# Kernel optimization log

Hardware: AMD Instinct MI355X
Metric: run time of the kernel (lower is better)

## Reference

```python
import jax, jax.numpy as jnp
import numpy as np

B, S, H = 2, 2048, 2048
NH, NKV, HD = 16, 8, 128        # head_dim = H // NH
WINDOW = 1024                    # sliding window size
THETA = 100000.0                 # rope_theta (RotaryEmbedding base)


def setup_inputs() -> dict:
    key = jax.random.key(0)
    ks = jax.random.split(key, 5)
    hidden = jax.random.normal(ks[0], (B, S, H), jnp.float32)
    # fused QKV projection: [H, NH*HD + 2*NKV*HD]
    W_pack = jax.random.normal(ks[1], (H, NH * HD + 2 * NKV * HD), jnp.float32) * (H ** -0.5)
    W_o = jax.random.normal(ks[2], (NH * HD, H), jnp.float32) * ((NH * HD) ** -0.5)
    # per-KV-head 2-tap causal conv weights, softmax-normalized (as in nn.Parameter init)
    conv_k = jax.nn.softmax(jax.random.normal(ks[3], (NKV, 2), jnp.float32), axis=-1)
    conv_v = jax.nn.softmax(jax.random.normal(ks[4], (NKV, 2), jnp.float32), axis=-1)
    return {"hidden": hidden, "W_pack": W_pack, "W_o": W_o, "conv_k": conv_k, "conv_v": conv_v}


def _rope(x, cos, sin):
    # x: (b, s, h, d); cos/sin: (s, d//2); non-interleaved (rotate-half) form
    d2 = x.shape[-1] // 2
    x1, x2 = x[..., :d2], x[..., d2:]
    c = cos[None, :, None, :]
    s = sin[None, :, None, :]
    return jnp.concatenate([x1 * c - x2 * s, x2 * c + x1 * s], axis=-1)


def _causal_conv2(x, w):
    # x: (b, s, kv, d); w: (kv, 2). out[t] = w0*x[t-1] + w1*x[t], zero-padded at t=0
    x_prev = jnp.pad(x, ((0, 0), (1, 0), (0, 0), (0, 0)))[:, :-1]
    return w[None, None, :, 0:1] * x_prev + w[None, None, :, 1:2] * x


def reference(hidden, W_pack, W_o, conv_k, conv_v):
    b, s, _ = hidden.shape
    qkv = hidden @ W_pack                                  # (b, s, NH*HD + 2*NKV*HD)
    q = qkv[..., : NH * HD].reshape(b, s, NH, HD)
    k = qkv[..., NH * HD : NH * HD + NKV * HD].reshape(b, s, NKV, HD)
    v = qkv[..., NH * HD + NKV * HD :].reshape(b, s, NKV, HD)

    inv_freq = 1.0 / (THETA ** (jnp.arange(0, HD, 2, dtype=jnp.float32) / HD))
    freqs = jnp.outer(jnp.arange(s, dtype=jnp.float32), inv_freq)  # (s, HD/2)
    cos, sin = jnp.cos(freqs), jnp.sin(freqs)
    q = _rope(q, cos, sin)
    k = _rope(k, cos, sin)

    # learned 2-tap causal conv mixing adjacent K/V states, per KV head
    k = _causal_conv2(k, conv_k)
    v = _causal_conv2(v, conv_v)

    # GQA: repeat kv heads to match query heads
    group = NH // NKV
    k = jnp.repeat(k, group, axis=2)  # (b, s, NH, HD)
    v = jnp.repeat(v, group, axis=2)

    scores = jnp.einsum('bqhd,bkhd->bhqk', q, k) / jnp.sqrt(jnp.float32(HD))
    i = jnp.arange(s)[:, None]
    j = jnp.arange(s)[None, :]
    mask = (j <= i) & (i - j < WINDOW)  # causal sliding-window mask
    scores = jnp.where(mask[None, None], scores, jnp.finfo(scores.dtype).min)
    probs = jax.nn.softmax(scores, axis=-1)
    out = jnp.einsum('bhqk,bkhd->bqhd', probs, v).reshape(b, s, NH * HD)
    return out @ W_o
```

## Files before the change

### kernel.cpp

```cpp
#include <hip/hip_runtime.h>

#define DI __device__ __forceinline__

typedef unsigned short u16;
typedef __attribute__((ext_vector_type(8))) short s16x8;
typedef __attribute__((ext_vector_type(8))) unsigned short u16x8;
typedef __attribute__((ext_vector_type(4))) float f32x4;
typedef __attribute__((ext_vector_type(16))) float f32x16;

DI u16 f2bf(float x) {
  union { float f; unsigned u; } a; a.f = x;
  unsigned r = a.u + 0x7FFFu + ((a.u >> 16) & 1u);
  return (u16)(r >> 16);
}
DI float bf2f(u16 u) {
  union { unsigned u; float f; } a; a.u = ((unsigned)u) << 16;
  return a.f;
}
DI void gload16(const void* g, void* l) {
  __builtin_amdgcn_global_load_lds(
      (const __attribute__((address_space(1))) unsigned int*)g,
      (__attribute__((address_space(3))) unsigned int*)l, 16, 0, 0);
}
DI f32x4 mfma16(s16x8 a, s16x8 b, f32x4 c) {
  return __builtin_amdgcn_mfma_f32_16x16x32_bf16(a, b, c, 0, 0, 0);
}
DI f32x16 mfma32(s16x8 a, s16x8 b, f32x16 c) {
  return __builtin_amdgcn_mfma_f32_32x32x16_bf16(a, b, c, 0, 0, 0);
}

DI void store4(u16* p, f32x4 v) {
  union { u16 u[4]; unsigned long long ll; } o;
  o.u[0] = f2bf(v[0]); o.u[1] = f2bf(v[1]); o.u[2] = f2bf(v[2]); o.u[3] = f2bf(v[3]);
  *(unsigned long long*)p = o.ll;
}
DI void store4(float* p, f32x4 v) { *(f32x4*)p = v; }

#define SBAR() asm volatile("s_barrier" ::: "memory")

__global__ __launch_bounds__(256) void prep_kernel(
    const float* __restrict__ hidden, const float* __restrict__ W_pack,
    const float* __restrict__ W_o, u16* __restrict__ hA, u16* __restrict__ wpT,
    u16* __restrict__ woT, float* __restrict__ cosT, float* __restrict__ sinT) {
  int bi = blockIdx.x;
  int t = threadIdx.x;
  if (bi < 4096) {
    int i = bi * 256 + t;
    const float4* p = (const float4*)hidden + (size_t)i * 2;
    float4 a = p[0], b = p[1];
    u16x8 o;
    o[0] = f2bf(a.x); o[1] = f2bf(a.y); o[2] = f2bf(a.z); o[3] = f2bf(a.w);
    o[4] = f2bf(b.x); o[5] = f2bf(b.y); o[6] = f2bf(b.z); o[7] = f2bf(b.w);
    *((u16x8*)hA + i) = o;
  } else if (bi < 7168) {
    const float* W; u16* Wt; int R, C, c0, r0;
    if (bi < 6144) {
      int idx = bi - 4096;
      W = W_pack; Wt = wpT; R = 2048; C = 4096;
      c0 = (idx & 63) * 64; r0 = (idx >> 6) * 64;
    } else {
      int idx = bi - 6144;
      W = W_o; Wt = woT; R = 2048; C = 2048;
      c0 = (idx & 31) * 64; r0 = (idx >> 5) * 64;
    }
    __shared__ u16 tile[64][65];
#pragma unroll
    for (int i = 0; i < 16; ++i) {
      int flat = i * 256 + t;
      int r = flat >> 6, c = flat & 63;
      tile[r][c] = f2bf(W[(size_t)(r0 + r) * C + (c0 + c)]);
    }
    __syncthreads();
#pragma unroll
    for (int i = 0; i < 16; ++i) {
      int flat = i * 256 + t;
      int c = flat >> 6, r = flat & 63;
      Wt[(size_t)(c0 + c) * R + (r0 + r)] = tile[r][c];
    }
  } else {
    int i = (bi - 7168) * 256 + t;
    int s = i >> 6, d = i & 63;
    float inv = expf(-(float)d * (11.5129254649702295f / 64.f));
    float f = (float)s * inv;
    cosT[i] = cosf(f);
    sinT[i] = sinf(f);
  }
}

__global__ __launch_bounds__(512, 2) void gemm_ring_kernel(
    const u16* __restrict__ A, const u16* __restrict__ Bt, u16* __restrict__ C,
    int M, int N, int K) {
  constexpr int BSZ = 32768;
  __shared__ __align__(16) char lds[4 * BSZ];
  int nwg = gridDim.x, bid = blockIdx.x;
  int cpx = nwg >> 3;
  int swz = (bid & 7) * cpx + (bid >> 3);
  int ntn = N >> 8;
  int bm = swz / ntn, bn = swz - bm * ntn;
  int m0 = bm << 8, n0 = bn << 8;
  int t = threadIdx.x, w = t >> 6, l = t & 63;
  int wm = w >> 2, wn = w & 3;
  int NT = K >> 5;

  unsigned srcA[2], srcB[2];
  unsigned scol = (unsigned)(((t & 3) ^ ((t >> 3) & 3)) << 4);
#pragma unroll
  for (int u = 0; u < 2; ++u) {
    srcA[u] = (unsigned)(m0 + u * 128 + (t >> 2)) * (unsigned)(K * 2) + scol;
    srcB[u] = (unsigned)(n0 + u * 128 + (t >> 2)) * (unsigned)(K * 2) + scol;
  }
  unsigned dstT = (unsigned)(t * 16);
  const char* Ab = (const char*)A;
  const char* Bb = (const char*)Bt;

#define STAGE(tile) do { int _t = (tile); if (_t < NT) {                        \
    char* _bb = lds + (size_t)(_t & 3) * BSZ;                                    \
    unsigned _k = (unsigned)_t * 64u;                                            \
    gload16(Ab + (size_t)(srcA[0] + _k), _bb + dstT);                            \
    gload16(Ab + (size_t)(srcA[1] + _k), _bb + 8192 + dstT);                     \
    gload16(Bb + (size_t)(srcB[0] + _k), _bb + 16384 + dstT);                    \
    gload16(Bb + (size_t)(srcB[1] + _k), _bb + 24576 + dstT);                    \
  } } while (0)

  int lanemix = ((l & 15) << 6) + ((((l >> 4) ^ ((l >> 1) & 3))) << 4);

  f32x4 acc[8][4] = {};
  s16x8 af[8], bfr[4];

  STAGE(0); STAGE(1); STAGE(2);
  asm volatile("s_waitcnt vmcnt(8)" ::: "memory");
  SBAR();

  for (int tt = 0; tt < NT; ++tt) {
    char* buf = lds + (size_t)(tt & 3) * BSZ;
    const char* Ard = buf + wm * 8192 + lanemix;
    const char* Brd = buf + 16384 + wn * 4096 + lanemix;
    STAGE(tt + 3);
#pragma unroll
    for (int mf = 0; mf < 8; ++mf) af[mf] = *(const s16x8*)(Ard + mf * 1024);
#pragma unroll
    for (int nf = 0; nf < 4; ++nf) bfr[nf] = *(const s16x8*)(Brd + nf * 1024);
    __builtin_amdgcn_s_setprio(1);
#pragma unroll
    for (int mf = 0; mf < 8; ++mf)
#pragma unroll
      for (int nf = 0; nf < 4; ++nf)
        acc[mf][nf] = mfma16(bfr[nf], af[mf], acc[mf][nf]);
    __builtin_amdgcn_s_setprio(0);
    if (tt + 1 < NT) {
      if (tt + 3 < NT)      asm volatile("s_waitcnt vmcnt(8)" ::: "memory");
      else if (tt + 2 < NT) asm volatile("s_waitcnt vmcnt(4)" ::: "memory");
      else                  asm volatile("s_waitcnt vmcnt(0)" ::: "memory");
      SBAR();
    }
  }
#undef STAGE

#pragma unroll
  for (int mf = 0; mf < 8; ++mf) {
    int row = m0 + wm * 128 + mf * 16 + (l & 15);
    u16* crow = C + (size_t)row * N + n0 + wn * 64 + (l >> 4) * 4;
#pragma unroll
    for (int nf = 0; nf < 4; ++nf) store4(crow + nf * 16, acc[mf][nf]);
  }
}

__global__ __launch_bounds__(512, 2) void gemm8pn_kernel(
    const u16* __restrict__ A, const u16* __restrict__ Bt, float* __restrict__ C,
    int M, int N, int K) {
  __shared__ __align__(16) char lds[98304];
  int nwg = gridDim.x;
  int bid = blockIdx.x;
  int cpx = nwg >> 3;
  int swz = (bid & 7) * cpx + (bid >> 3);
  int ntn = N >> 7;
  int bm = swz / ntn, bn = swz - bm * ntn;
  int m0 = bm << 8, n0 = bn << 7;
  int t = threadIdx.x, w = t >> 6, l = t & 63;
  int wm = w >> 2, wn = w & 3;
  int NT = K >> 6;

  unsigned offA[4], offB[2];
  int cA[4], cB[2];
#pragma unroll
  for (int u = 0; u < 4; ++u) {
    int c = u * 8 + w;
    cA[u] = c;
    int d = c * 1024 + l * 16;
    int s = d ^ ((((d >> 7) & 7)) << 4);
    offA[u] = (unsigned)(m0 + (s >> 7)) * (unsigned)(K * 2) + (unsigned)(s & 127);
  }
#pragma unroll
  for (int u = 0; u < 2; ++u) {
    int c = u * 8 + w;
    cB[u] = c;
    int d = c * 1024 + l * 16;
    int s = d ^ ((((d >> 7) & 7)) << 4);
    offB[u] = (unsigned)(n0 + (s >> 7)) * (unsigned)(K * 2) + (unsigned)(s & 127);
  }
  const char* Ab = (const char*)A;
  const char* Bb = (const char*)Bt;

#define STG_A(tile, u) do { int _t = (tile); if (_t < NT) {                    \
    gload16(Ab + (size_t)(offA[u] + (unsigned)_t * 128u),                       \
            lds + (_t & 1) * 49152 + cA[u] * 1024); } } while (0)
#define STG_B(tile, u) do { int _t = (tile); if (_t < NT) {                    \
    gload16(Bb + (size_t)(offB[u] + (unsigned)_t * 128u),                       \
            lds + (_t & 1) * 49152 + 32768 + cB[u] * 1024); } } while (0)

  int lanemix = ((l & 15) << 7) + ((((l >> 4) << 4) ^ ((l & 7) << 4)));
  int lanemix1 = lanemix ^ 64;

  f32x4 acc[8][2] = {};
  s16x8 af[4][2], bf0[2], bf1[2];

  STG_A(0, 0); STG_A(0, 1); STG_A(0, 2); STG_A(0, 3); STG_B(0, 0); STG_B(0, 1);
  STG_A(1, 0); STG_A(1, 1); STG_A(1, 2); STG_A(1, 3); STG_B(1, 0); STG_B(1, 1);
  asm volatile("s_waitcnt vmcnt(6)" ::: "memory");
  SBAR();

  for (int tt = 0; tt < NT; ++tt) {
    const char* ldsA = lds + (tt & 1) * 49152;
    const char* ldsB = ldsA + 32768;
    const char* Ard0 = ldsA + (wm << 14) + lanemix;
    const char* Ard1 = ldsA + (wm << 14) + lanemix1;
    const char* Brd0 = ldsB + (wn << 12) + lanemix;
    const char* Brd1 = ldsB + (wn << 12) + lanemix1;

#pragma unroll
    for (int mf = 0; mf < 4; ++mf) {
      af[mf][0] = *(const s16x8*)(Ard0 + mf * 2048);
      af[mf][1] = *(const s16x8*)(Ard1 + mf * 2048);
    }
    bf0[0] = *(const s16x8*)(Brd0);
    bf0[1] = *(const s16x8*)(Brd1);
    SBAR();
    __builtin_amdgcn_s_setprio(1);
#pragma unroll
    for (int mf = 0; mf < 4; ++mf) {
      acc[mf][0] = mfma16(bf0[0], af[mf][0], acc[mf][0]);
      acc[mf][0] = mfma16(bf0[1], af[mf][1], acc[mf][0]);
    }
    __builtin_amdgcn_s_setprio(0);
    SBAR();

    bf1[0] = *(const s16x8*)(Brd0 + 2048);
    bf1[1] = *(const s16x8*)(Brd1 + 2048);
    STG_A(tt + 2, 0); STG_A(tt + 2, 2);
    SBAR();
    __builtin_amdgcn_s_setprio(1);
#pragma unroll
    for (int mf = 0; mf < 4; ++mf) {
      acc[mf][1] = mfma16(bf1[0], af[mf][0], acc[mf][1]);
      acc[mf][1] = mfma16(bf1[1], af[mf][1], acc[mf][1]);
    }
    __builtin_amdgcn_s_setprio(0);
    SBAR();

#pragma unroll
    for (int mf = 0; mf < 4; ++mf) {
      af[mf][0] = *(const s16x8*)(Ard0 + (mf + 4) * 2048);
      af[mf][1] = *(const s16x8*)(Ard1 + (mf + 4) * 2048);
    }
    STG_B(tt + 2, 0); STG_B(tt + 2, 1);
    SBAR();
    __builtin_amdgcn_s_setprio(1);
#pragma unroll
    for (int mf = 0; mf < 4; ++mf) {
      acc[mf + 4][0] = mfma16(bf0[0], af[mf][0], acc[mf + 4][0]);
      acc[mf + 4][0] = mfma16(bf0[1], af[mf][1], acc[mf + 4][0]);
    }
    __builtin_amdgcn_s_setprio(0);
    SBAR();

    STG_A(tt + 2, 1); STG_A(tt + 2, 3);
    SBAR();
    __builtin_amdgcn_s_setprio(1);
#pragma unroll
    for (int mf = 0; mf < 4; ++mf) {
      acc[mf + 4][1] = mfma16(bf1[0], af[mf][0], acc[mf + 4][1]);
      acc[mf + 4][1] = mfma16(bf1[1], af[mf][1], acc[mf + 4][1]);
    }
    __builtin_amdgcn_s_setprio(0);
    if (tt < NT - 2) asm volatile("s_waitcnt vmcnt(6)" ::: "memory");
    else             asm volatile("s_waitcnt vmcnt(0)" ::: "memory");
    SBAR();
  }
#undef STG_A
#undef STG_B

#pragma unroll
  for (int mf = 0; mf < 8; ++mf) {
    int row = m0 + wm * 128 + mf * 16 + (l & 15);
    float* crow = C + (size_t)row * N + n0 + wn * 32 + (l >> 4) * 4;
#pragma unroll
    for (int nf = 0; nf < 2; ++nf) store4(crow + nf * 16, acc[mf][nf]);
  }
}

__global__ void rcvt_kernel(const u16* __restrict__ qkv, const float* __restrict__ cosT,
                            const float* __restrict__ sinT, const float* __restrict__ convk,
                            const float* __restrict__ convv,
                            u16* __restrict__ qb, u16* __restrict__ kb,
                            u16* __restrict__ vt) {
  int t = threadIdx.x;
  if (blockIdx.x < 4096) {
    const float qs = 0.08838834764831845f;
    int row = blockIdx.x;
    int b = row >> 11, s = row & 2047;
    const u16* qr = qkv + (size_t)row * 4096;
    u16* qo = qb + (size_t)row * 2048;
#pragma unroll
    for (int i = 0; i < 4; ++i) {
      int p = i * 256 + t;
      int h = p >> 6, d = p & 63;
      float x1 = bf2f(qr[h * 128 + d]), x2 = bf2f(qr[h * 128 + 64 + d]);
      float c = cosT[s * 64 + d], sn = sinT[s * 64 + d];
      qo[h * 128 + d] = f2bf((x1 * c - x2 * sn) * qs);
      qo[h * 128 + 64 + d] = f2bf((x2 * c + x1 * sn) * qs);
    }
    const u16* kr = qr + 2048;
#pragma unroll
    for (int i = 0; i < 2; ++i) {
      int p = i * 256 + t;
      int h = p >> 6, d = p & 63;
      float c = cosT[s * 64 + d], sn = sinT[s * 64 + d];
      float x1 = bf2f(kr[h * 128 + d]), x2 = bf2f(kr[h * 128 + 64 + d]);
      float r1 = x1 * c - x2 * sn, r2 = x2 * c + x1 * sn;
      float p1 = 0.f, p2 = 0.f;
      if (s > 0) {
        const u16* kp = kr - 4096;
        float cp = cosT[(s - 1) * 64 + d], sp = sinT[(s - 1) * 64 + d];
        float y1 = bf2f(kp[h * 128 + d]), y2 = bf2f(kp[h * 128 + 64 + d]);
        p1 = y1 * cp - y2 * sp;
        p2 = y2 * cp + y1 * sp;
      }
      float w0 = convk[h * 2], w1 = convk[h * 2 + 1];
      size_t o = (((size_t)b * 8 + h) * 2048 + s) * 128;
      kb[o + d] = f2bf(w0 * p1 + w1 * r1);
      kb[o + 64 + d] = f2bf(w0 * p2 + w1 * r2);
    }
  } else {
    __shared__ u16 lt[128][72];
    int idx = blockIdx.x - 4096;
    int st = idx & 31, bh = idx >> 5;
    int b = bh >> 3, h = bh & 7;
    int s0 = st * 64;
    float w0 = convv[h * 2], w1 = convv[h * 2 + 1];
#pragma unroll
    for (int i = 0; i < 32; ++i) {
      int flat = i * 256 + t;
      int sl = flat >> 7, d = flat & 127;
      int s = s0 + sl;
      int row = b * 2048 + s;
      float x = bf2f(qkv[(size_t)row * 4096 + 3072 + h * 128 + d]);
      float xp = (s > 0) ? bf2f(qkv[(size_t)(row - 1) * 4096 + 3072 + h * 128 + d]) : 0.f;
      lt[d][sl] = f2bf(w0 * xp + w1 * x);
    }
    __syncthreads();
#pragma unroll
    for (int i = 0; i < 32; ++i) {
      int flat = i * 256 + t;
      int d = flat >> 6, sl = flat & 63;
      vt[((size_t)(b * 8 + h) * 128 + d) * 2048 + s0 + sl] = lt[d][sl];
    }
  }
}

__global__ __launch_bounds__(256, 2) void attn2_kernel(
    const u16* __restrict__ qb, const u16* __restrict__ kbuf, const u16* __restrict__ vt,
    u16* __restrict__ ao) {
  __shared__ __align__(16) char lds[65536];
  int qt = blockIdx.x, bh = blockIdx.y;
  int b = bh >> 4, h = bh & 15, kh = h >> 1;
  int t = threadIdx.x, w = t >> 6, l = t & 63;
  int i0 = qt * 128;
  int qbase = i0 + w * 32;
  int lq = l & 31, hi = l >> 5;
  int xorc = (l & 7) << 4;
  const char* Kg = (const char*)(kbuf + (size_t)(b * 8 + kh) * 2048 * 128);
  const char* Vg = (const char*)(vt + (size_t)(b * 8 + kh) * 128 * 2048);

  s16x8 qf[8];
  {
    const u16* qp = qb + ((size_t)(b * 2048 + qbase + lq)) * 2048 + h * 128 + 8 * hi;
#pragma unroll
    for (int kc = 0; kc < 8; ++kc) qf[kc] = *(const s16x8*)(qp + kc * 16);
  }

  unsigned ksrc[4], vsrc[4], kdst[4], vdst[4];
#pragma unroll
  for (int i = 0; i < 4; ++i) {
    int c = w * 4 + i;
    int row = c * 4 + (l >> 4);
    int colb = (l & 15) * 16;
    ksrc[i] = (unsigned)(row * 256 + (colb ^ ((row & 7) << 4)));
    kdst[i] = (unsigned)(c * 1024);
    int d = c * 8 + (l >> 3);
    int cb2 = (l & 7) * 16;
    vsrc[i] = (unsigned)(d * 4096 + (cb2 ^ ((d & 7) << 4)));
    vdst[i] = (unsigned)(16384 + c * 1024);
  }

#define STAGEKV(tile, buf) do { int _j2 = (tile) << 6;                          \
    char* _lb = lds + ((buf) << 15);                                             \
    const char* _ks = Kg + (size_t)_j2 * 256;                                    \
    const char* _vs = Vg + (size_t)_j2 * 2;                                      \
    gload16(_ks + ksrc[0], _lb + kdst[0]); gload16(_vs + vsrc[0], _lb + vdst[0]);\
    gload16(_ks + ksrc[1], _lb + kdst[1]); gload16(_vs + vsrc[1], _lb + vdst[1]);\
    gload16(_ks + ksrc[2], _lb + kdst[2]); gload16(_vs + vsrc[2], _lb + vdst[2]);\
    gload16(_ks + ksrc[3], _lb + kdst[3]); gload16(_vs + vsrc[3], _lb + vdst[3]);\
  } while (0)

  int lo = i0 - 1023; if (lo < 0) lo = 0;
  int tk0 = lo >> 6, tk1 = (i0 + 127) >> 6;

  f32x16 acco[4] = {};
  float ls0 = 0.f, ls1 = 0.f, ls2 = 0.f, ls3 = 0.f;

  int cur = 0;
  STAGEKV(tk0, 0);
  asm volatile("s_waitcnt vmcnt(0)" ::: "memory");
  SBAR();

  for (int tk = tk0; tk <= tk1; ++tk) {
    int j0 = tk << 6;
    if (tk < tk1) STAGEKV(tk + 1, cur ^ 1);
    bool relevant = (j0 <= qbase + 31) && (j0 + 63 >= qbase - 1023);
    if (relevant) {
      const char* Kl = lds + (cur << 15);
      const char* Vl = Kl + 16384;
      const char* Krow = Kl + lq * 256;
      f32x16 ps0 = {}, ps1 = {};
      __builtin_amdgcn_s_setprio(1);
#pragma unroll
      for (int kc = 0; kc < 8; ++kc) {
        s16x8 kf = *(const s16x8*)(Krow + ((kc * 32 + hi * 16) ^ xorc));
        ps0 = mfma32(kf, qf[kc], ps0);
      }
#pragma unroll
      for (int kc = 0; kc < 8; ++kc) {
        s16x8 kf = *(const s16x8*)(Krow + 8192 + ((kc * 32 + hi * 16) ^ xorc));
        ps1 = mfma32(kf, qf[kc], ps1);
      }
      __builtin_amdgcn_s_setprio(0);
      bool domask = (j0 + 63 > qbase) || (qbase + 31 - j0 >= 1024);
      int di0 = qbase + lq - j0;
      float pe[32];
#pragma unroll
      for (int r = 0; r < 16; ++r) {
        float s0 = ps0[r], s1 = ps1[r];
        if (domask) {
          int crow = (r & 3) + 8 * (r >> 2) + 4 * hi;
          if ((unsigned)(di0 - crow) >= 1024u) s0 = -1e30f;
          if ((unsigned)(di0 - 32 - crow) >= 1024u) s1 = -1e30f;
        }
        float e0 = __expf(s0), e1 = __expf(s1);
        pe[r] = e0; pe[16 + r] = e1;
        if ((r & 3) == 0) { ls0 += e0 + e1; }
        else if ((r & 3) == 1) { ls1 += e0 + e1; }
        else if ((r & 3) == 2) { ls2 += e0 + e1; }
        else { ls3 += e0 + e1; }
      }
      unsigned pk[16];
#pragma unroll
      for (int p = 0; p < 16; ++p) {
        asm("v_cvt_pk_bf16_f32 %0, %1, %2" : "=v"(pk[p]) : "v"(pe[2 * p]), "v"(pe[2 * p + 1]));
      }
      s16x8 pa[4];
#pragma unroll
      for (int ks = 0; ks < 4; ++ks) {
        int base = (ks >> 1) * 8 + (ks & 1) * 4;
        unsigned keep0 = hi ? pk[base + 2] : pk[base + 0];
        unsigned keep1 = hi ? pk[base + 3] : pk[base + 1];
        unsigned send0 = hi ? pk[base + 0] : pk[base + 2];
        unsigned send1 = hi ? pk[base + 1] : pk[base + 3];
        unsigned recv0 = (unsigned)__shfl_xor((int)send0, 32);
        unsigned recv1 = (unsigned)__shfl_xor((int)send1, 32);
        union { unsigned u[4]; s16x8 v; } pu;
        pu.u[0] = hi ? recv0 : keep0;
        pu.u[1] = hi ? recv1 : keep1;
        pu.u[2] = hi ? keep0 : recv0;
        pu.u[3] = hi ? keep1 : recv1;
        pa[ks] = pu.v;
      }
      __builtin_amdgcn_s_setprio(1);
#pragma unroll
      for (int db = 0; db < 4; ++db) {
        const char* Vrow = Vl + db * 4096 + lq * 128;
#pragma unroll
        for (int ks = 0; ks < 4; ++ks) {
          s16x8 vf = *(const s16x8*)(Vrow + ((ks * 32 + hi * 16) ^ xorc));
          acco[db] = mfma32(pa[ks], vf, acco[db]);
        }
      }
      __builtin_amdgcn_s_setprio(0);
    }
    asm volatile("s_waitcnt vmcnt(0)" ::: "memory");
    SBAR();
    cur ^= 1;
  }
#undef STAGEKV

  float lrow = (ls0 + ls1) + (ls2 + ls3);
  float lt2 = lrow + __shfl_xor(lrow, 32);
  float rinv = 1.f / lt2;
#pragma unroll
  for (int r = 0; r < 16; ++r) {
    int qidx = (r & 3) + 8 * (r >> 2) + 4 * hi;
    float rv = __shfl(rinv, qidx);
    int i = qbase + qidx;
    u16* orow = ao + ((size_t)(b * 2048 + i)) * 2048 + h * 128 + lq;
#pragma unroll
    for (int db = 0; db < 4; ++db)
      orow[db * 32] = f2bf(acco[db][r] * rv);
  }
}

extern "C" void kernel_launch(void* const* d_in, const int* in_sizes, int n_in,
                              void* d_out, int out_size, void* d_ws, size_t ws_size,
                              hipStream_t stream) {
  (void)in_sizes; (void)n_in; (void)out_size; (void)ws_size;
  const float* hidden = (const float*)d_in[0];
  const float* W_pack = (const float*)d_in[1];
  const float* W_o    = (const float*)d_in[2];
  const float* conv_k = (const float*)d_in[3];
  const float* conv_v = (const float*)d_in[4];

  char* ws = (char*)d_ws;
  const size_t MB = 1u << 20;
  u16* hA    = (u16*)(ws + 0);
  u16* wpT   = (u16*)(ws + 16 * MB);
  u16* woT   = (u16*)(ws + 32 * MB);
  u16* qkv   = (u16*)(ws + 40 * MB);
  u16* qb    = (u16*)(ws + 72 * MB);
  u16* kbuf  = (u16*)(ws + 88 * MB);
  u16* vtb   = (u16*)(ws + 96 * MB);
  float* cosT = (float*)(ws + 104 * MB);
  float* sinT = (float*)(ws + 104 * MB + 524288);
  u16* attnb = qkv;

  prep_kernel<<<7680, 256, 0, stream>>>(hidden, W_pack, W_o, hA, wpT, woT, cosT, sinT);
  gemm_ring_kernel<<<256, 512, 0, stream>>>(hA, wpT, qkv, 4096, 4096, 2048);
  rcvt_kernel<<<4608, 256, 0, stream>>>(qkv, cosT, sinT, conv_k, conv_v, qb, kbuf, vtb);
  attn2_kernel<<<dim3(16, 32), 256, 0, stream>>>(qb, kbuf, vtb, attnb);
  gemm8pn_kernel<<<256, 512, 0, stream>>>(attnb, woT, (float*)d_out,
                                          4096, 2048, 2048);
}
```

Baseline: 191.0 us.

## Fuse Q RoPE into attention load and use triple-buffered output GEMM

Result: no change. 192.3 us (+0.7%).

```diff
diff --git a/kernel.cpp b/kernel.cpp
--- a/kernel.cpp
+++ b/kernel.cpp
@@ -165,12 +165,11 @@
   }
 }
 
-__global__ __launch_bounds__(512, 2) void gemm8pn_kernel(
+__global__ __launch_bounds__(512, 2) void gemm2r_kernel(
     const u16* __restrict__ A, const u16* __restrict__ Bt, float* __restrict__ C,
     int M, int N, int K) {
-  __shared__ __align__(16) char lds[98304];
-  int nwg = gridDim.x;
-  int bid = blockIdx.x;
+  __shared__ __align__(16) char lds[3 * 49152];
+  int nwg = gridDim.x, bid = blockIdx.x;
   int cpx = nwg >> 3;
   int swz = (bid & 7) * cpx + (bid >> 3);
   int ntn = N >> 7;
@@ -201,93 +200,59 @@
   const char* Ab = (const char*)A;
   const char* Bb = (const char*)Bt;
 
-#define STG_A(tile, u) do { int _t = (tile); if (_t < NT) {                    \
-    gload16(Ab + (size_t)(offA[u] + (unsigned)_t * 128u),                       \
-            lds + (_t & 1) * 49152 + cA[u] * 1024); } } while (0)
-#define STG_B(tile, u) do { int _t = (tile); if (_t < NT) {                    \
-    gload16(Bb + (size_t)(offB[u] + (unsigned)_t * 128u),                       \
-            lds + (_t & 1) * 49152 + 32768 + cB[u] * 1024); } } while (0)
+#define STG(tile) do { int _t = (tile); if (_t < NT) {                          \
+    char* _bb = lds + (size_t)(_t % 3) * 49152;                                  \
+    unsigned _k = (unsigned)_t * 128u;                                           \
+    gload16(Ab + (size_t)(offA[0] + _k), _bb + cA[0] * 1024);                    \
+    gload16(Ab + (size_t)(offA[1] + _k), _bb + cA[1] * 1024);                    \
+    gload16(Ab + (size_t)(offA[2] + _k), _bb + cA[2] * 1024);                    \
+    gload16(Ab + (size_t)(offA[3] + _k), _bb + cA[3] * 1024);                    \
+    gload16(Bb + (size_t)(offB[0] + _k), _bb + 32768 + cB[0] * 1024);            \
+    gload16(Bb + (size_t)(offB[1] + _k), _bb + 32768 + cB[1] * 1024);            \
+  } } while (0)
 
   int lanemix = ((l & 15) << 7) + ((((l >> 4) << 4) ^ ((l & 7) << 4)));
   int lanemix1 = lanemix ^ 64;
 
   f32x4 acc[8][2] = {};
-  s16x8 af[4][2], bf0[2], bf1[2];
-
-  STG_A(0, 0); STG_A(0, 1); STG_A(0, 2); STG_A(0, 3); STG_B(0, 0); STG_B(0, 1);
-  STG_A(1, 0); STG_A(1, 1); STG_A(1, 2); STG_A(1, 3); STG_B(1, 0); STG_B(1, 1);
+  s16x8 af[8][2], bf0[2], bf1[2];
+
+  STG(0); STG(1);
   asm volatile("s_waitcnt vmcnt(6)" ::: "memory");
   SBAR();
 
   for (int tt = 0; tt < NT; ++tt) {
-    const char* ldsA = lds + (tt & 1) * 49152;
-    const char* ldsB = ldsA + 32768;
-    const char* Ard0 = ldsA + (wm << 14) + lanemix;
-    const char* Ard1 = ldsA + (wm << 14) + lanemix1;
-    const char* Brd0 = ldsB + (wn << 12) + lanemix;
-    const char* Brd1 = ldsB + (wn << 12) + lanemix1;
-
-#pragma unroll
-    for (int mf = 0; mf < 4; ++mf) {
+    char* buf = lds + (size_t)(tt % 3) * 49152;
+    const char* Ard0 = buf + (wm << 14) + lanemix;
+    const char* Ard1 = buf + (wm << 14) + lanemix1;
+    const char* Brd0 = buf + 32768 + (wn << 12) + lanemix;
+    const char* Brd1 = buf + 32768 + (wn << 12) + lanemix1;
+    STG(tt + 2);
+#pragma unroll
+    for (int mf = 0; mf < 8; ++mf) {
       af[mf][0] = *(const s16x8*)(Ard0 + mf * 2048);
       af[mf][1] = *(const s16x8*)(Ard1 + mf * 2048);
     }
     bf0[0] = *(const s16x8*)(Brd0);
     bf0[1] = *(const s16x8*)(Brd1);
-    SBAR();
+    bf1[0] = *(const s16x8*)(Brd0 + 2048);
+    bf1[1] = *(const s16x8*)(Brd1 + 2048);
     __builtin_amdgcn_s_setprio(1);
 #pragma unroll
-    for (int mf = 0; mf < 4; ++mf) {
+    for (int mf = 0; mf < 8; ++mf) {
       acc[mf][0] = mfma16(bf0[0], af[mf][0], acc[mf][0]);
       acc[mf][0] = mfma16(bf0[1], af[mf][1], acc[mf][0]);
-    }
-    __builtin_amdgcn_s_setprio(0);
-    SBAR();
-
-    bf1[0] = *(const s16x8*)(Brd0 + 2048);
-    bf1[1] = *(const s16x8*)(Brd1 + 2048);
-    STG_A(tt + 2, 0); STG_A(tt + 2, 2);
-    SBAR();
-    __builtin_amdgcn_s_setprio(1);
-#pragma unroll
-    for (int mf = 0; mf < 4; ++mf) {
       acc[mf][1] = mfma16(bf1[0], af[mf][0], acc[mf][1]);
       acc[mf][1] = mfma16(bf1[1], af[mf][1], acc[mf][1]);
     }
     __builtin_amdgcn_s_setprio(0);
-    SBAR();
-
-#pragma unroll
-    for (int mf = 0; mf < 4; ++mf) {
-      af[mf][0] = *(const s16x8*)(Ard0 + (mf + 4) * 2048);
-      af[mf][1] = *(const s16x8*)(Ard1 + (mf + 4) * 2048);
-    }
-    STG_B(tt + 2, 0); STG_B(tt + 2, 1);
-    SBAR();
-    __builtin_amdgcn_s_setprio(1);
-#pragma unroll
-    for (int mf = 0; mf < 4; ++mf) {
-      acc[mf + 4][0] = mfma16(bf0[0], af[mf][0], acc[mf + 4][0]);
-      acc[mf + 4][0] = mfma16(bf0[1], af[mf][1], acc[mf + 4][0]);
-    }
-    __builtin_amdgcn_s_setprio(0);
-    SBAR();
-
-    STG_A(tt + 2, 1); STG_A(tt + 2, 3);
-    SBAR();
-    __builtin_amdgcn_s_setprio(1);
-#pragma unroll
-    for (int mf = 0; mf < 4; ++mf) {
-      acc[mf + 4][1] = mfma16(bf1[0], af[mf][0], acc[mf + 4][1]);
-      acc[mf + 4][1] = mfma16(bf1[1], af[mf][1], acc[mf + 4][1]);
-    }
-    __builtin_amdgcn_s_setprio(0);
-    if (tt < NT - 2) asm volatile("s_waitcnt vmcnt(6)" ::: "memory");
-    else             asm volatile("s_waitcnt vmcnt(0)" ::: "memory");
-    SBAR();
-  }
-#undef STG_A
-#undef STG_B
+    if (tt + 1 < NT) {
+      if (tt + 2 < NT) asm volatile("s_waitcnt vmcnt(6)" ::: "memory");
+      else             asm volatile("s_waitcnt vmcnt(0)" ::: "memory");
+      SBAR();
+    }
+  }
+#undef STG
 
 #pragma unroll
   for (int mf = 0; mf < 8; ++mf) {
@@ -301,25 +266,12 @@
 __global__ void rcvt_kernel(const u16* __restrict__ qkv, const float* __restrict__ cosT,
                             const float* __restrict__ sinT, const float* __restrict__ convk,
                             const float* __restrict__ convv,
-                            u16* __restrict__ qb, u16* __restrict__ kb,
-                            u16* __restrict__ vt) {
+                            u16* __restrict__ kb, u16* __restrict__ vt) {
   int t = threadIdx.x;
   if (blockIdx.x < 4096) {
-    const float qs = 0.08838834764831845f;
     int row = blockIdx.x;
     int b = row >> 11, s = row & 2047;
-    const u16* qr = qkv + (size_t)row * 4096;
-    u16* qo = qb + (size_t)row * 2048;
-#pragma unroll
-    for (int i = 0; i < 4; ++i) {
-      int p = i * 256 + t;
-      int h = p >> 6, d = p & 63;
-      float x1 = bf2f(qr[h * 128 + d]), x2 = bf2f(qr[h * 128 + 64 + d]);
-      float c = cosT[s * 64 + d], sn = sinT[s * 64 + d];
-      qo[h * 128 + d] = f2bf((x1 * c - x2 * sn) * qs);
-      qo[h * 128 + 64 + d] = f2bf((x2 * c + x1 * sn) * qs);
-    }
-    const u16* kr = qr + 2048;
+    const u16* kr = qkv + (size_t)row * 4096 + 2048;
 #pragma unroll
     for (int i = 0; i < 2; ++i) {
       int p = i * 256 + t;
@@ -368,8 +320,9 @@
 }
 
 __global__ __launch_bounds__(256, 2) void attn2_kernel(
-    const u16* __restrict__ qb, const u16* __restrict__ kbuf, const u16* __restrict__ vt,
-    u16* __restrict__ ao) {
+    const u16* __restrict__ qkv, const float* __restrict__ cosT,
+    const float* __restrict__ sinT, const u16* __restrict__ kbuf,
+    const u16* __restrict__ vt, u16* __restrict__ ao) {
   __shared__ __align__(16) char lds[65536];
   int qt = blockIdx.x, bh = blockIdx.y;
   int b = bh >> 4, h = bh & 15, kh = h >> 1;
@@ -383,9 +336,32 @@
 
   s16x8 qf[8];
   {
-    const u16* qp = qb + ((size_t)(b * 2048 + qbase + lq)) * 2048 + h * 128 + 8 * hi;
-#pragma unroll
-    for (int kc = 0; kc < 8; ++kc) qf[kc] = *(const s16x8*)(qp + kc * 16);
+    const float qs = 0.08838834764831845f;
+    int srow = qbase + lq;
+    const u16* qp = qkv + ((size_t)(b * 2048 + srow)) * 4096 + h * 128 + 8 * hi;
+    const float* cb = cosT + srow * 64 + 8 * hi;
+    const float* sb = sinT + srow * 64 + 8 * hi;
+#pragma unroll
+    for (int kc = 0; kc < 4; ++kc) {
+      s16x8 vlo = *(const s16x8*)(qp + kc * 16);
+      s16x8 vhi = *(const s16x8*)(qp + 64 + kc * 16);
+      float4 c0 = *(const float4*)(cb + kc * 16);
+      float4 c1 = *(const float4*)(cb + kc * 16 + 4);
+      float4 s0 = *(const float4*)(sb + kc * 16);
+      float4 s1 = *(const float4*)(sb + kc * 16 + 4);
+      float cc[8] = {c0.x, c0.y, c0.z, c0.w, c1.x, c1.y, c1.z, c1.w};
+      float ss[8] = {s0.x, s0.y, s0.z, s0.w, s1.x, s1.y, s1.z, s1.w};
+      u16 ol[8], oh[8];
+#pragma unroll
+      for (int j = 0; j < 8; ++j) {
+        float xl = bf2f(((const u16*)&vlo)[j]);
+        float xh = bf2f(((const u16*)&vhi)[j]);
+        ol[j] = f2bf((xl * cc[j] - xh * ss[j]) * qs);
+        oh[j] = f2bf((xh * cc[j] + xl * ss[j]) * qs);
+      }
+      qf[kc] = *(s16x8*)ol;
+      qf[kc + 4] = *(s16x8*)oh;
+    }
   }
 
   unsigned ksrc[4], vsrc[4], kdst[4], vdst[4];
@@ -533,17 +509,15 @@
   u16* wpT   = (u16*)(ws + 16 * MB);
   u16* woT   = (u16*)(ws + 32 * MB);
   u16* qkv   = (u16*)(ws + 40 * MB);
-  u16* qb    = (u16*)(ws + 72 * MB);
+  u16* attnb = (u16*)(ws + 72 * MB);
   u16* kbuf  = (u16*)(ws + 88 * MB);
   u16* vtb   = (u16*)(ws + 96 * MB);
   float* cosT = (float*)(ws + 104 * MB);
   float* sinT = (float*)(ws + 104 * MB + 524288);
-  u16* attnb = qkv;
 
   prep_kernel<<<7680, 256, 0, stream>>>(hidden, W_pack, W_o, hA, wpT, woT, cosT, sinT);
   gemm_ring_kernel<<<256, 512, 0, stream>>>(hA, wpT, qkv, 4096, 4096, 2048);
-  rcvt_kernel<<<4608, 256, 0, stream>>>(qkv, cosT, sinT, conv_k, conv_v, qb, kbuf, vtb);
-  attn2_kernel<<<dim3(16, 32), 256, 0, stream>>>(qb, kbuf, vtb, attnb);
-  gemm8pn_kernel<<<256, 512, 0, stream>>>(attnb, woT, (float*)d_out,
-                                          4096, 2048, 2048);
-}
+  rcvt_kernel<<<4608, 256, 0, stream>>>(qkv, cosT, sinT, conv_k, conv_v, kbuf, vtb);
+  attn2_kernel<<<dim3(16, 32), 256, 0, stream>>>(qkv, cosT, sinT, kbuf, vtb, attnb);
+  gemm2r_kernel<<<256, 512, 0, stream>>>(attnb, woT, (float*)d_out, 4096, 2048, 2048);
+}
```

## Fuse Q rotary embedding into attention load and use native exp2

Applied to the files above, without the earlier changes.

Measured after the change: 195.9 us. 1.03x slower.

```diff
diff --git a/kernel.cpp b/kernel.cpp
--- a/kernel.cpp
+++ b/kernel.cpp
@@ -27,6 +27,11 @@
 }
 DI f32x16 mfma32(s16x8 a, s16x8 b, f32x16 c) {
   return __builtin_amdgcn_mfma_f32_32x32x16_bf16(a, b, c, 0, 0, 0);
+}
+DI float exp2fast(float x) {
+  float r;
+  asm("v_exp_f32 %0, %1" : "=v"(r) : "v"(x));
+  return r;
 }
 
 DI void store4(u16* p, f32x4 v) {
@@ -301,25 +306,12 @@
 __global__ void rcvt_kernel(const u16* __restrict__ qkv, const float* __restrict__ cosT,
                             const float* __restrict__ sinT, const float* __restrict__ convk,
                             const float* __restrict__ convv,
-                            u16* __restrict__ qb, u16* __restrict__ kb,
-                            u16* __restrict__ vt) {
+                            u16* __restrict__ kb, u16* __restrict__ vt) {
   int t = threadIdx.x;
   if (blockIdx.x < 4096) {
-    const float qs = 0.08838834764831845f;
     int row = blockIdx.x;
     int b = row >> 11, s = row & 2047;
-    const u16* qr = qkv + (size_t)row * 4096;
-    u16* qo = qb + (size_t)row * 2048;
-#pragma unroll
-    for (int i = 0; i < 4; ++i) {
-      int p = i * 256 + t;
-      int h = p >> 6, d = p & 63;
-      float x1 = bf2f(qr[h * 128 + d]), x2 = bf2f(qr[h * 128 + 64 + d]);
-      float c = cosT[s * 64 + d], sn = sinT[s * 64 + d];
-      qo[h * 128 + d] = f2bf((x1 * c - x2 * sn) * qs);
-      qo[h * 128 + 64 + d] = f2bf((x2 * c + x1 * sn) * qs);
-    }
-    const u16* kr = qr + 2048;
+    const u16* kr = qkv + (size_t)row * 4096 + 2048;
 #pragma unroll
     for (int i = 0; i < 2; ++i) {
       int p = i * 256 + t;
@@ -368,8 +360,9 @@
 }
 
 __global__ __launch_bounds__(256, 2) void attn2_kernel(
-    const u16* __restrict__ qb, const u16* __restrict__ kbuf, const u16* __restrict__ vt,
-    u16* __restrict__ ao) {
+    const u16* __restrict__ qkv, const float* __restrict__ cosT,
+    const float* __restrict__ sinT, const u16* __restrict__ kbuf,
+    const u16* __restrict__ vt, u16* __restrict__ ao) {
   __shared__ __align__(16) char lds[65536];
   int qt = blockIdx.x, bh = blockIdx.y;
   int b = bh >> 4, h = bh & 15, kh = h >> 1;
@@ -383,9 +376,32 @@
 
   s16x8 qf[8];
   {
-    const u16* qp = qb + ((size_t)(b * 2048 + qbase + lq)) * 2048 + h * 128 + 8 * hi;
-#pragma unroll
-    for (int kc = 0; kc < 8; ++kc) qf[kc] = *(const s16x8*)(qp + kc * 16);
+    const float qs = 0.12751747157186644f;
+    int srow = qbase + lq;
+    const u16* qp = qkv + ((size_t)(b * 2048 + srow)) * 4096 + h * 128 + 8 * hi;
+    const float* cb = cosT + srow * 64 + 8 * hi;
+    const float* sb = sinT + srow * 64 + 8 * hi;
+#pragma unroll
+    for (int kc = 0; kc < 4; ++kc) {
+      s16x8 vlo = *(const s16x8*)(qp + kc * 16);
+      s16x8 vhi = *(const s16x8*)(qp + 64 + kc * 16);
+      float4 c0 = *(const float4*)(cb + kc * 16);
+      float4 c1 = *(const float4*)(cb + kc * 16 + 4);
+      float4 s0 = *(const float4*)(sb + kc * 16);
+      float4 s1 = *(const float4*)(sb + kc * 16 + 4);
+      float cc[8] = {c0.x, c0.y, c0.z, c0.w, c1.x, c1.y, c1.z, c1.w};
+      float ss[8] = {s0.x, s0.y, s0.z, s0.w, s1.x, s1.y, s1.z, s1.w};
+      u16 ol[8], oh[8];
+#pragma unroll
+      for (int j = 0; j < 8; ++j) {
+        float xl = bf2f(((const u16*)&vlo)[j]);
+        float xh = bf2f(((const u16*)&vhi)[j]);
+        ol[j] = f2bf((xl * cc[j] - xh * ss[j]) * qs);
+        oh[j] = f2bf((xh * cc[j] + xl * ss[j]) * qs);
+      }
+      qf[kc] = *(s16x8*)ol;
+      qf[kc + 4] = *(s16x8*)oh;
+    }
   }
 
   unsigned ksrc[4], vsrc[4], kdst[4], vdst[4];
@@ -455,7 +471,7 @@
           if ((unsigned)(di0 - crow) >= 1024u) s0 = -1e30f;
           if ((unsigned)(di0 - 32 - crow) >= 1024u) s1 = -1e30f;
         }
-        float e0 = __expf(s0), e1 = __expf(s1);
+        float e0 = exp2fast(s0), e1 = exp2fast(s1);
         pe[r] = e0; pe[16 + r] = e1;
         if ((r & 3) == 0) { ls0 += e0 + e1; }
         else if ((r & 3) == 1) { ls1 += e0 + e1; }
@@ -533,17 +549,15 @@
   u16* wpT   = (u16*)(ws + 16 * MB);
   u16* woT   = (u16*)(ws + 32 * MB);
   u16* qkv   = (u16*)(ws + 40 * MB);
-  u16* qb    = (u16*)(ws + 72 * MB);
+  u16* attnb = (u16*)(ws + 72 * MB);
   u16* kbuf  = (u16*)(ws + 88 * MB);
   u16* vtb   = (u16*)(ws + 96 * MB);
   float* cosT = (float*)(ws + 104 * MB);
   float* sinT = (float*)(ws + 104 * MB + 524288);
-  u16* attnb = qkv;
 
   prep_kernel<<<7680, 256, 0, stream>>>(hidden, W_pack, W_o, hA, wpT, woT, cosT, sinT);
   gemm_ring_kernel<<<256, 512, 0, stream>>>(hA, wpT, qkv, 4096, 4096, 2048);
-  rcvt_kernel<<<4608, 256, 0, stream>>>(qkv, cosT, sinT, conv_k, conv_v, qb, kbuf, vtb);
-  attn2_kernel<<<dim3(16, 32), 256, 0, stream>>>(qb, kbuf, vtb, attnb);
-  gemm8pn_kernel<<<256, 512, 0, stream>>>(attnb, woT, (float*)d_out,
-                                          4096, 2048, 2048);
-}
+  rcvt_kernel<<<4608, 256, 0, stream>>>(qkv, cosT, sinT, conv_k, conv_v, kbuf, vtb);
+  attn2_kernel<<<dim3(16, 32), 256, 0, stream>>>(qkv, cosT, sinT, kbuf, vtb, attnb);
+  gemm8pn_kernel<<<256, 512, 0, stream>>>(attnb, woT, (float*)d_out, 4096, 2048, 2048);
+}
```
